# Kernel optimization log

Measured on AMD Instinct MI355X. Metric: run time of the kernel, lower is better.

## Reference

```python
import jax, jax.numpy as jnp
import numpy as np

B, H, W = 4, 1024, 1024

# 8-tap Sobel-style stencil: offsets in (u, v) units of (dx, dy)
OFF_U = jnp.array([-1.0, -1.0, -1.0, 0.0, 0.0, 1.0, 1.0, 1.0], dtype=jnp.float32)
OFF_V = jnp.array([-1.0, 0.0, 1.0, -1.0, 1.0, -1.0, 0.0, 1.0], dtype=jnp.float32)
KU = jnp.array([-0.25, -0.5, -0.25, 0.0, 0.0, 0.25, 0.5, 0.25], dtype=jnp.float32)
KV = jnp.array([-0.25, 0.0, 0.25, -0.5, 0.5, -0.25, 0.0, 0.25], dtype=jnp.float32)


def setup_inputs() -> dict:
    key = jax.random.key(0)
    k1, k2 = jax.random.split(key)
    x = jax.random.uniform(k1, (B, 3, H, W), dtype=jnp.float32)
    sigma = jax.random.uniform(k2, (B,), dtype=jnp.float32) * 2.0 + 0.5  # pixels
    return {"x": x, "sigma": sigma}


def _bilinear(tex, u, v):
    # tex: [3, H, W]; u, v: [8, H, W] normalized UV in [0,1]
    Hh, Ww = tex.shape[1], tex.shape[2]
    px = u * Ww - 0.5
    py = v * Hh - 0.5
    x0 = jnp.floor(px)
    y0 = jnp.floor(py)
    fx = (px - x0)[None]  # [1,8,H,W]
    fy = (py - y0)[None]
    x0i = jnp.clip(x0.astype(jnp.int32), 0, Ww - 1)
    x1i = jnp.clip(x0i + 1, 0, Ww - 1)
    y0i = jnp.clip(y0.astype(jnp.int32), 0, Hh - 1)
    y1i = jnp.clip(y0i + 1, 0, Hh - 1)
    t00 = tex[:, y0i, x0i]  # [3,8,H,W]
    t01 = tex[:, y0i, x1i]
    t10 = tex[:, y1i, x0i]
    t11 = tex[:, y1i, x1i]
    return (t00 * (1 - fx) * (1 - fy) + t01 * fx * (1 - fy)
            + t10 * (1 - fx) * fy + t11 * fx * fy)


def reference(x, sigma):
    Bb, C, Hh, Ww = x.shape
    ys, xs = jnp.meshgrid(jnp.arange(Hh, dtype=x.dtype),
                          jnp.arange(Ww, dtype=x.dtype), indexing='ij')
    u0 = (xs + 0.5) / Ww  # pixel-center UV
    v0 = (ys + 0.5) / Hh
    dx = sigma / Ww  # [B]
    dy = sigma / Hh
    u = u0[None, None] + OFF_U[None, :, None, None] * dx[:, None, None, None]  # [B,8,H,W]
    v = v0[None, None] + OFF_V[None, :, None, None] * dy[:, None, None, None]
    s = jax.vmap(_bilinear)(x, u, v)  # [B,3,8,H,W]
    s_u = jnp.einsum('bcthw,t->bchw', s, KU)
    s_v = jnp.einsum('bcthw,t->bchw', s, KV)
    lum = jnp.array([100.0, 1.0, 1.0], dtype=x.dtype)[None, :, None, None]
    s_u = s_u * lum
    s_v = s_v * lum
    # structure tensor components E, G, F
    return jnp.stack([(s_u * s_u).sum(1), (s_v * s_v).sum(1), (s_u * s_v).sum(1)], axis=1)
```

## Files before the change

kernel.cpp:

```cpp
#include <hip/hip_runtime.h>


#define W_ 1024
#define H_ 1024
#define PLANE (1 << 20)
#define TCOLS 64
#define TROWS 32
#define ROWS 8
#define LSTRIDE 72

__device__ __forceinline__ float lerp1(float a, float b, float f) {
    return fmaf(f, b - a, a);
}

__device__ __forceinline__ void async_copy16(const float* g, float* s) {
    __builtin_amdgcn_global_load_lds(
        (const __attribute__((address_space(1))) unsigned int*)g,
        (__attribute__((address_space(3))) unsigned int*)s,
        16, 0, 0);
}

__device__ void slow_pixel(const float* __restrict__ Xb, float* __restrict__ Ob,
                           float sg, int xi, int y)
{
    float imf = floorf(-sg), ipf = floorf(sg);
    float fm  = -sg - imf;
    float fp  =  sg - ipf;
    int   im  = (int)imf, ip = (int)ipf;

    int cm0 = min(max(xi + im, 0), W_ - 1), cm1 = min(cm0 + 1, W_ - 1);
    int cp0 = min(max(xi + ip, 0), W_ - 1), cp1 = min(cp0 + 1, W_ - 1);
    int rm0 = min(max(y + im, 0), H_ - 1),  rm1 = min(rm0 + 1, H_ - 1);
    int rp0 = min(max(y + ip, 0), H_ - 1),  rp1 = min(rp0 + 1, H_ - 1);

    int o_rm0 = rm0 << 10, o_rm1 = rm1 << 10;
    int o_rp0 = rp0 << 10, o_rp1 = rp1 << 10;
    int o_r0  = y   << 10;

    float oxx = 0.f, oyy = 0.f, oxy = 0.f;

    #pragma unroll
    for (int c = 0; c < 3; ++c) {
        const float* base = Xb + ((size_t)c << 20);

        float hm_m0 = lerp1(base[o_rm0 + cm0], base[o_rm0 + cm1], fm);
        float hm_m1 = lerp1(base[o_rm1 + cm0], base[o_rm1 + cm1], fm);
        float hm_0  = lerp1(base[o_r0  + cm0], base[o_r0  + cm1], fm);
        float hm_p0 = lerp1(base[o_rp0 + cm0], base[o_rp0 + cm1], fm);
        float hm_p1 = lerp1(base[o_rp1 + cm0], base[o_rp1 + cm1], fm);
        float hp_m0 = lerp1(base[o_rm0 + cp0], base[o_rm0 + cp1], fp);
        float hp_m1 = lerp1(base[o_rm1 + cp0], base[o_rm1 + cp1], fp);
        float hp_0  = lerp1(base[o_r0  + cp0], base[o_r0  + cp1], fp);
        float hp_p0 = lerp1(base[o_rp0 + cp0], base[o_rp0 + cp1], fp);
        float hp_p1 = lerp1(base[o_rp1 + cp0], base[o_rp1 + cp1], fp);
        float h0_m0 = base[o_rm0 + xi], h0_m1 = base[o_rm1 + xi];
        float h0_p0 = base[o_rp0 + xi], h0_p1 = base[o_rp1 + xi];

        float t0 = lerp1(hm_m0, hm_m1, fm);
        float t1 = hm_0;
        float t2 = lerp1(hm_p0, hm_p1, fp);
        float t3 = lerp1(h0_m0, h0_m1, fm);
        float t4 = lerp1(h0_p0, h0_p1, fp);
        float t5 = lerp1(hp_m0, hp_m1, fm);
        float t6 = hp_0;
        float t7 = lerp1(hp_p0, hp_p1, fp);

        float su = 0.25f * (t5 + t7 - t0 - t2) + 0.5f * (t6 - t1);
        float sv = 0.25f * (t2 + t7 - t0 - t5) + 0.5f * (t4 - t3);

        float l2 = (c == 0) ? 10000.f : 1.f;
        oxx = fmaf(l2 * su, su, oxx);
        oyy = fmaf(l2 * sv, sv, oyy);
        oxy = fmaf(l2 * su, sv, oxy);
    }

    int pix = (y << 10) | xi;
    Ob[pix]             = oxx;
    Ob[PLANE + pix]     = oyy;
    Ob[2 * PLANE + pix] = oxy;
}

template<int N>
__device__ __forceinline__ void acc(float (&arr)[N], int k, float val) {
    if (k >= 0 && k < N) arr[k] += val;
}

template<int IP>
__device__ void fast_tile(const float* __restrict__ Xb, float* __restrict__ Ob,
                          float fp, float fm, int x0, int y0,
                          int tx, int ty, int tid, float* smem)
{
    constexpr int LROWS  = TROWS + 2 * IP + 2;
    constexpr int RW     = ROWS + 2 * IP + 2;
    constexpr int NG     = 3 * LROWS * 18;
    constexpr int FULLIT = NG / 256;

    int x = x0 + tx;
    int Y = y0 + ty * ROWS;

    auto stage = [&](int g) {
        int row  = g / 18;
        int grp  = g - row * 18;
        int c    = row / LROWS;
        int lrow = row - c * LROWS;
        int gr   = min(max(y0 - IP - 1 + lrow, 0), H_ - 1);
        int gc   = min(max(x0 - 4 + grp * 4, 0), W_ - 4);
        async_copy16(Xb + ((size_t)c << 20) + (gr << 10) + gc,
                     smem + g * 4);
    };

    #pragma unroll
    for (int it = 0; it < FULLIT; ++it)
        stage(it * 256 + tid);
    if (FULLIT * 256 + tid < NG)
        stage(FULLIT * 256 + tid);

    __syncthreads();

    float oxx[ROWS], oyy[ROWS], oxy[ROWS];
    #pragma unroll
    for (int k = 0; k < ROWS; ++k) { oxx[k] = 0.f; oyy[k] = 0.f; oxy[k] = 0.f; }

    const float* spb = smem + (ty * ROWS) * LSTRIDE + tx + (3 - IP);

    #pragma unroll
    for (int c = 0; c < 3; ++c) {
        const float* sp = spb + c * (LROWS * LSTRIDE);

        float su[ROWS], sv[ROWS];
        #pragma unroll
        for (int k = 0; k < ROWS; ++k) { su[k] = 0.f; sv[k] = 0.f; }

        #pragma unroll
        for (int w = 0; w < RW; ++w) {
            float a0 = sp[w * LSTRIDE];
            float a1 = sp[w * LSTRIDE + 1];
            float cc = sp[w * LSTRIDE + IP + 1];
            float b0 = sp[w * LSTRIDE + 2 * IP + 1];
            float b1 = sp[w * LSTRIDE + 2 * IP + 2];
            float hm = lerp1(a0, a1, fm);
            float hp = lerp1(b0, b1, fp);
            float q  = hp - hm;
            float A  = 0.25f * q;
            float hq = 0.5f  * q;
            float Bv = fmaf(0.25f, hm + hp, 0.5f * cc);
            float fpA = fp * A,  fmA = fm * A;
            float fpB = fp * Bv, fmB = fm * Bv;

            acc(su, w,              fpA);
            acc(su, w - 1,          fmA);
            acc(su, w - IP - 1,     hq);
            acc(su, w - 2*IP - 1,   fmA);
            acc(su, w - 2*IP - 2,   fpA);
            acc(sv, w,             -fpB);
            acc(sv, w - 1,         -fmB);
            acc(sv, w - 2*IP - 1,   fmB);
            acc(sv, w - 2*IP - 2,   fpB);
        }

        float l2 = (c == 0) ? 10000.f : 1.f;
        #pragma unroll
        for (int k = 0; k < ROWS; ++k) {
            oxx[k] = fmaf(l2 * su[k], su[k], oxx[k]);
            oyy[k] = fmaf(l2 * sv[k], sv[k], oyy[k]);
            oxy[k] = fmaf(l2 * su[k], sv[k], oxy[k]);
        }
    }

    bool okx = (x > IP) && (x < W_ - 1 - IP);
    #pragma unroll
    for (int k = 0; k < ROWS; ++k) {
        int y = Y + k;
        if (okx && y > IP) {
            int pix = (y << 10) | x;
            Ob[pix]             = oxx[k];
            Ob[PLANE + pix]     = oyy[k];
            Ob[2 * PLANE + pix] = oxy[k];
        }
    }
}

__global__ __launch_bounds__(256) void st_kernel(
    const float* __restrict__ X, const float* __restrict__ S,
    float* __restrict__ O)
{
    int b  = blockIdx.z;
    const float* Xb = X + (size_t)b * 3 * PLANE;
    float*       Ob = O + (size_t)b * 3 * PLANE;
    float sg = S[b];

    int tx = threadIdx.x, ty = threadIdx.y;
    int tid = ty * 64 + tx;

    if (blockIdx.y == 0) {
        int t = blockIdx.x * 256 + tid;
        #pragma unroll
        for (int it = 0; it < 3; ++it) {
            int pidx = t + it * 4096;
            if (pidx < 6144) {
                int yy = pidx / 6;
                int cc = pidx - yy * 6;
                int xx = (cc < 3) ? cc : (W_ - 6 + cc);
                slow_pixel(Xb, Ob, sg, xx, yy);
            } else if (pidx < 9216) {
                int p2 = pidx - 6144;
                slow_pixel(Xb, Ob, sg, p2 & 1023, p2 >> 10);
            }
        }
        return;
    }

    int x0 = blockIdx.x * TCOLS;
    int y0 = (blockIdx.y - 1) * TROWS;

    int ipv = (int)floorf(sg);
    int imv = (int)floorf(-sg);
    bool sig_ok = (imv == -ipv - 1) && ipv >= 0 && ipv <= 2;
    float fp = sg - (float)ipv;
    float fm = 1.0f - fp;

    __shared__ float smem[3 * (TROWS + 6) * LSTRIDE];

    if (sig_ok) {
        switch (ipv) {
            case 0:  fast_tile<0>(Xb, Ob, fp, fm, x0, y0, tx, ty, tid, smem); break;
            case 1:  fast_tile<1>(Xb, Ob, fp, fm, x0, y0, tx, ty, tid, smem); break;
            default: fast_tile<2>(Xb, Ob, fp, fm, x0, y0, tx, ty, tid, smem); break;
        }
    } else {
        for (int k = 0; k < ROWS; ++k)
            slow_pixel(Xb, Ob, sg, x0 + tx, y0 + ty * ROWS + k);
    }
}

extern "C" void kernel_launch(void* const* d_in, const int* in_sizes, int n_in,
                              void* d_out, int out_size, void* d_ws, size_t ws_size,
                              hipStream_t stream) {
    const float* x     = (const float*)d_in[0];
    const float* sigma = (const float*)d_in[1];
    float* out = (float*)d_out;

    dim3 grid(W_ / TCOLS, H_ / TROWS + 1, 4), block(64, 4);
    hipLaunchKernelGGL(st_kernel, grid, block, 0, stream, x, sigma, out);
}
```

Before: 113.0 us.

## Process four row tiles per block with double-buffered async LDS staging

Each block now walks four consecutive 32-row tiles. It double-buffers the LDS input: the next tile is prefetched with async global-to-LDS copies while the current tile is computed, synchronised by manual vmcnt waits and barriers. This aims to hide global load latency behind stencil compute and cut per-block launch overhead. In exchange the grid has a quarter as many blocks, LDS use doubles (which may lower occupancy), and correctness relies on hand-tuned vmcnt counts matching the number of issued loads.

```diff
diff --git a/kernel.cpp b/kernel.cpp
--- a/kernel.cpp
+++ b/kernel.cpp
@@ -8,6 +8,8 @@
 #define TROWS 32
 #define ROWS 8
 #define LSTRIDE 72
+#define NTILES 4
+#define BUFSZ 9232
 
 __device__ __forceinline__ float lerp1(float a, float b, float f) {
     return fmaf(f, b - a, a);
@@ -86,97 +88,111 @@
 }
 
 template<int IP>
-__device__ void fast_tile(const float* __restrict__ Xb, float* __restrict__ Ob,
-                          float fp, float fm, int x0, int y0,
-                          int tx, int ty, int tid, float* smem)
+__device__ void fast_tiles(const float* __restrict__ Xb, float* __restrict__ Ob,
+                           float fp, float fm, int x0, int band0,
+                           int tx, int ty, int tid, float* smem)
 {
-    constexpr int LROWS  = TROWS + 2 * IP + 2;
-    constexpr int RW     = ROWS + 2 * IP + 2;
-    constexpr int NG     = 3 * LROWS * 18;
-    constexpr int FULLIT = NG / 256;
+    constexpr int LROWS = TROWS + 2 * IP + 2;
+    constexpr int RW    = ROWS + 2 * IP + 2;
+    constexpr int NG    = 3 * LROWS * 18;
+    constexpr int ITERS = (NG + 255) / 256;
 
     int x = x0 + tx;
-    int Y = y0 + ty * ROWS;
-
-    auto stage = [&](int g) {
-        int row  = g / 18;
-        int grp  = g - row * 18;
-        int c    = row / LROWS;
-        int lrow = row - c * LROWS;
-        int gr   = min(max(y0 - IP - 1 + lrow, 0), H_ - 1);
-        int gc   = min(max(x0 - 4 + grp * 4, 0), W_ - 4);
-        async_copy16(Xb + ((size_t)c << 20) + (gr << 10) + gc,
-                     smem + g * 4);
+
+    auto stage = [&](float* buf, int y0) {
+        #pragma unroll
+        for (int it = 0; it < ITERS; ++it) {
+            int g    = min(it * 256 + tid, NG - 1);
+            int row  = g / 18;
+            int grp  = g - row * 18;
+            int c    = row / LROWS;
+            int lrow = row - c * LROWS;
+            int gr   = min(max(y0 - IP - 1 + lrow, 0), H_ - 1);
+            int gc   = min(max(x0 - 4 + grp * 4, 0), W_ - 4);
+            async_copy16(Xb + ((size_t)c << 20) + (gr << 10) + gc,
+                         buf + g * 4);
+        }
     };
 
+    stage(smem,         (band0 + 0) * TROWS);
+    stage(smem + BUFSZ, (band0 + 1) * TROWS);
+
     #pragma unroll
-    for (int it = 0; it < FULLIT; ++it)
-        stage(it * 256 + tid);
-    if (FULLIT * 256 + tid < NG)
-        stage(FULLIT * 256 + tid);
-
-    __syncthreads();
-
-    float oxx[ROWS], oyy[ROWS], oxy[ROWS];
-    #pragma unroll
-    for (int k = 0; k < ROWS; ++k) { oxx[k] = 0.f; oyy[k] = 0.f; oxy[k] = 0.f; }
-
-    const float* spb = smem + (ty * ROWS) * LSTRIDE + tx + (3 - IP);
-
-    #pragma unroll
-    for (int c = 0; c < 3; ++c) {
-        const float* sp = spb + c * (LROWS * LSTRIDE);
-
-        float su[ROWS], sv[ROWS];
-        #pragma unroll
-        for (int k = 0; k < ROWS; ++k) { su[k] = 0.f; sv[k] = 0.f; }
-
-        #pragma unroll
-        for (int w = 0; w < RW; ++w) {
-            float a0 = sp[w * LSTRIDE];
-            float a1 = sp[w * LSTRIDE + 1];
-            float cc = sp[w * LSTRIDE + IP + 1];
-            float b0 = sp[w * LSTRIDE + 2 * IP + 1];
-            float b1 = sp[w * LSTRIDE + 2 * IP + 2];
-            float hm = lerp1(a0, a1, fm);
-            float hp = lerp1(b0, b1, fp);
-            float q  = hp - hm;
-            float A  = 0.25f * q;
-            float hq = 0.5f  * q;
-            float Bv = fmaf(0.25f, hm + hp, 0.5f * cc);
-            float fpA = fp * A,  fmA = fm * A;
-            float fpB = fp * Bv, fmB = fm * Bv;
-
-            acc(su, w,              fpA);
-            acc(su, w - 1,          fmA);
-            acc(su, w - IP - 1,     hq);
-            acc(su, w - 2*IP - 1,   fmA);
-            acc(su, w - 2*IP - 2,   fpA);
-            acc(sv, w,             -fpB);
-            acc(sv, w - 1,         -fmB);
-            acc(sv, w - 2*IP - 1,   fmB);
-            acc(sv, w - 2*IP - 2,   fpB);
-        }
-
-        float l2 = (c == 0) ? 10000.f : 1.f;
+    for (int t = 0; t < NTILES; ++t) {
+        float* buf = smem + (t & 1) * BUFSZ;
+        int y0 = (band0 + t) * TROWS;
+
+        if constexpr (ITERS >= 9) asm volatile("s_waitcnt vmcnt(9)" ::: "memory");
+        else                      asm volatile("s_waitcnt vmcnt(8)" ::: "memory");
+        __builtin_amdgcn_s_barrier();
+
+        float oxx[ROWS], oyy[ROWS], oxy[ROWS];
+        #pragma unroll
+        for (int k = 0; k < ROWS; ++k) { oxx[k] = 0.f; oyy[k] = 0.f; oxy[k] = 0.f; }
+
+        const float* spb = buf + (ty * ROWS) * LSTRIDE + tx + (3 - IP);
+
+        #pragma unroll
+        for (int c = 0; c < 3; ++c) {
+            const float* sp = spb + c * (LROWS * LSTRIDE);
+
+            float su[ROWS], sv[ROWS];
+            #pragma unroll
+            for (int k = 0; k < ROWS; ++k) { su[k] = 0.f; sv[k] = 0.f; }
+
+            #pragma unroll
+            for (int w = 0; w < RW; ++w) {
+                float a0 = sp[w * LSTRIDE];
+                float a1 = sp[w * LSTRIDE + 1];
+                float cc = sp[w * LSTRIDE + IP + 1];
+                float b0 = sp[w * LSTRIDE + 2 * IP + 1];
+                float b1 = sp[w * LSTRIDE + 2 * IP + 2];
+                float hm = lerp1(a0, a1, fm);
+                float hp = lerp1(b0, b1, fp);
+                float q  = hp - hm;
+                float A  = 0.25f * q;
+                float hq = 0.5f  * q;
+                float Bv = fmaf(0.25f, hm + hp, 0.5f * cc);
+                float fpA = fp * A,  fmA = fm * A;
+                float fpB = fp * Bv, fmB = fm * Bv;
+
+                acc(su, w,              fpA);
+                acc(su, w - 1,          fmA);
+                acc(su, w - IP - 1,     hq);
+                acc(su, w - 2*IP - 1,   fmA);
+                acc(su, w - 2*IP - 2,   fpA);
+                acc(sv, w,             -fpB);
+                acc(sv, w - 1,         -fmB);
+                acc(sv, w - 2*IP - 1,   fmB);
+                acc(sv, w - 2*IP - 2,   fpB);
+            }
+
+            float l2 = (c == 0) ? 10000.f : 1.f;
+            #pragma unroll
+            for (int k = 0; k < ROWS; ++k) {
+                oxx[k] = fmaf(l2 * su[k], su[k], oxx[k]);
+                oyy[k] = fmaf(l2 * sv[k], sv[k], oyy[k]);
+                oxy[k] = fmaf(l2 * su[k], sv[k], oxy[k]);
+            }
+        }
+
+        bool okx = (x > IP) && (x < W_ - 1 - IP);
+        int Y = y0 + ty * ROWS;
         #pragma unroll
         for (int k = 0; k < ROWS; ++k) {
-            oxx[k] = fmaf(l2 * su[k], su[k], oxx[k]);
-            oyy[k] = fmaf(l2 * sv[k], sv[k], oyy[k]);
-            oxy[k] = fmaf(l2 * su[k], sv[k], oxy[k]);
-        }
-    }
-
-    bool okx = (x > IP) && (x < W_ - 1 - IP);
-    #pragma unroll
-    for (int k = 0; k < ROWS; ++k) {
-        int y = Y + k;
-        if (okx && y > IP) {
-            int pix = (y << 10) | x;
-            Ob[pix]             = oxx[k];
-            Ob[PLANE + pix]     = oyy[k];
-            Ob[2 * PLANE + pix] = oxy[k];
-        }
+            int y = Y + k;
+            if (okx && y > IP) {
+                int pix = (y << 10) | x;
+                Ob[pix]             = oxx[k];
+                Ob[PLANE + pix]     = oyy[k];
+                Ob[2 * PLANE + pix] = oxy[k];
+            }
+        }
+
+        asm volatile("s_waitcnt lgkmcnt(0)" ::: "memory");
+        __builtin_amdgcn_s_barrier();
+        if (t + 2 < NTILES)
+            stage(buf, (band0 + t + 2) * TROWS);
     }
 }
 
@@ -210,8 +226,8 @@
         return;
     }
 
-    int x0 = blockIdx.x * TCOLS;
-    int y0 = (blockIdx.y - 1) * TROWS;
+    int x0    = blockIdx.x * TCOLS;
+    int band0 = (blockIdx.y - 1) * NTILES;
 
     int ipv = (int)floorf(sg);
     int imv = (int)floorf(-sg);
@@ -219,17 +235,19 @@
     float fp = sg - (float)ipv;
     float fm = 1.0f - fp;
 
-    __shared__ float smem[3 * (TROWS + 6) * LSTRIDE];
+    __shared__ __align__(16) float smem[2 * BUFSZ];
 
     if (sig_ok) {
         switch (ipv) {
-            case 0:  fast_tile<0>(Xb, Ob, fp, fm, x0, y0, tx, ty, tid, smem); break;
-            case 1:  fast_tile<1>(Xb, Ob, fp, fm, x0, y0, tx, ty, tid, smem); break;
-            default: fast_tile<2>(Xb, Ob, fp, fm, x0, y0, tx, ty, tid, smem); break;
+            case 0:  fast_tiles<0>(Xb, Ob, fp, fm, x0, band0, tx, ty, tid, smem); break;
+            case 1:  fast_tiles<1>(Xb, Ob, fp, fm, x0, band0, tx, ty, tid, smem); break;
+            default: fast_tiles<2>(Xb, Ob, fp, fm, x0, band0, tx, ty, tid, smem); break;
         }
     } else {
-        for (int k = 0; k < ROWS; ++k)
-            slow_pixel(Xb, Ob, sg, x0 + tx, y0 + ty * ROWS + k);
+        for (int t = 0; t < NTILES; ++t)
+            for (int k = 0; k < ROWS; ++k)
+                slow_pixel(Xb, Ob, sg, x0 + tx,
+                           (band0 + t) * TROWS + ty * ROWS + k);
     }
 }
 
@@ -240,6 +258,6 @@
     const float* sigma = (const float*)d_in[1];
     float* out = (float*)d_out;
 
-    dim3 grid(W_ / TCOLS, H_ / TROWS + 1, 4), block(64, 4);
+    dim3 grid(W_ / TCOLS, H_ / TROWS / NTILES + 1, 4), block(64, 4);
     hipLaunchKernelGGL(st_kernel, grid, block, 0, stream, x, sigma, out);
 }
```

New measurement: 113.1 us. No clear change (+0.0%).
